# Kernel optimization log

Measured on AMD Instinct MI355X. Metric: run time of the kernel, lower is better.

The kernel has to match this reference:

```python
import jax, jax.numpy as jnp
import numpy as np

M = 8192   # predicted boxes
N = 8192   # ground-truth boxes
W_CENTER, W_SIZE, W_IOU = 1.0, 0.5, 2.0
MATCH_THRESH = 5.0


def setup_inputs() -> dict:
    key = jax.random.key(0)
    k1, k2, k3, k4 = jax.random.split(key, 4)
    centers = jax.random.uniform(k1, (N, 3), dtype=jnp.float32) * 100.0
    sizes = jax.random.uniform(k2, (N, 3), dtype=jnp.float32) * 3.0 + 1.0
    yaw = jax.random.uniform(k3, (N, 1), dtype=jnp.float32) * (2.0 * jnp.pi) - jnp.pi
    gt_boxes = jnp.concatenate([centers, sizes, yaw], axis=1)  # [N,7]
    # preds = perturbed gts so the 5.0 m matching gate actually fires
    pred_boxes = gt_boxes + 0.5 * jax.random.normal(k4, (M, 7), dtype=jnp.float32)
    return {"pred_boxes": pred_boxes, "gt_boxes": gt_boxes}


def _greedy_match(pred_boxes, gt_boxes):
    """Sequential greedy nearest-center matching (torch loop -> lax.scan).
    Column deletion in the original is equivalent to masking with an
    availability vector: argmin over remaining columns with first-tie wins.
    Returns (mask [M] bool: pred i matched, idx [M] int: matched gt index)."""
    # [M,N] center distance matrix (the memory-heavy irregular part)
    diff = pred_boxes[:, None, :3] - gt_boxes[None, :, :3]
    dist = jnp.sqrt(jnp.sum(diff * diff, axis=-1))

    def step(avail, d_row):
        dm = jnp.where(avail, d_row, jnp.inf)
        j = jnp.argmin(dm)
        ok = dm[j] < MATCH_THRESH
        avail = avail.at[j].set(jnp.logical_and(avail[j], jnp.logical_not(ok)))
        return avail, (ok, j)

    avail0 = jnp.ones((gt_boxes.shape[0],), dtype=bool)
    _, (mask, idx) = jax.lax.scan(step, avail0, dist)
    return mask, idx


def _smooth_l1(x):
    a = jnp.abs(x)
    return jnp.where(a < 1.0, 0.5 * a * a, a - 0.5)


def _iou_2d(b1, b2):
    # axis-aligned BEV IoU using (x, y, l, w)
    x1, y1, l1, w1 = b1[:, 0], b1[:, 1], b1[:, 3], b1[:, 4]
    x2, y2, l2, w2 = b2[:, 0], b2[:, 1], b2[:, 3], b2[:, 4]
    iw = jnp.clip(jnp.minimum(x1 + l1 / 2, x2 + l2 / 2) - jnp.maximum(x1 - l1 / 2, x2 - l2 / 2), 0.0)
    ih = jnp.clip(jnp.minimum(y1 + w1 / 2, y2 + w2 / 2) - jnp.maximum(y1 - w1 / 2, y2 - w2 / 2), 0.0)
    inter = iw * ih
    union = l1 * w1 + l2 * w2 - inter
    return inter / (union + 1e-6)


def _loss(pred_boxes, gt_boxes, mask, idx):
    mg = gt_boxes[idx]                              # [M,7] matched gts
    m = mask.astype(pred_boxes.dtype)               # [M]
    k = jnp.maximum(jnp.sum(m), 1.0)                # number of matches
    loss_center = jnp.sum(m[:, None] * _smooth_l1(pred_boxes[:, :3] - mg[:, :3])) / (3.0 * k)
    loss_size = jnp.sum(m[:, None] * _smooth_l1(pred_boxes[:, 3:6] - mg[:, 3:6])) / (3.0 * k)
    d = pred_boxes[:, 6] - mg[:, 6]
    d = jnp.arctan2(jnp.sin(d), jnp.cos(d))         # wrap to (-pi, pi]
    loss_orient = jnp.sum(m * _smooth_l1(d)) / k
    loss_iou = jnp.sum(m * (1.0 - _iou_2d(pred_boxes, mg))) / k
    return W_CENTER * loss_center + W_SIZE * (loss_size + loss_orient) + W_IOU * loss_iou


def reference(pred_boxes, gt_boxes):
    mask, idx = _greedy_match(pred_boxes, gt_boxes)
    return _loss(pred_boxes, gt_boxes, mask, idx)
```

## Files before the change

### kernel.cpp

```cpp
#include <hip/hip_runtime.h>
#include <stdint.h>

#define MROWS 8192
#define NGT   8192
#define KC    8
#define KL    4
#define RPW   2
#define RPL   4
#define THRESH2_BITS 0x41C7FFFFu
#define THRESH_BITS  0x40A00000u

__device__ __forceinline__ unsigned dist2_bits(float px, float py, float pz,
                                               float gx, float gy, float gz) {
#pragma clang fp contract(off)
  float dx = px - gx;
  float dy = py - gy;
  float dz = pz - gz;
  float s = (dx * dx + dy * dy) + dz * dz;
  return __float_as_uint(s);
}

__device__ __forceinline__ unsigned long long wave_min64(unsigned long long v) {
#pragma unroll
  for (int off = 32; off >= 1; off >>= 1) {
    unsigned long long o = __shfl_xor(v, off, 64);
    v = (o < v) ? o : v;
  }
  return v;
}

template <int K>
__device__ __forceinline__ void insert_sorted(unsigned (&kd)[K], unsigned (&ki)[K],
                                              unsigned key, unsigned j) {
#pragma unroll
  for (int t = K - 1; t >= 1; --t) {
    bool a = key < kd[t];
    bool b = key < kd[t - 1];
    if (a) {
      if (b) { kd[t] = kd[t - 1]; ki[t] = ki[t - 1]; }
      else   { kd[t] = key;       ki[t] = j; }
    }
  }
  if (key < kd[0]) { kd[0] = key; ki[0] = j; }
}

template <int K>
__device__ __forceinline__ void extract8(unsigned (&kd)[K], unsigned (&ki)[K], int lane,
                                         unsigned& resd, unsigned& resi,
                                         unsigned long long& e8) {
#pragma unroll
  for (int rr = 0; rr < KC; ++rr) {
    unsigned long long head = ((unsigned long long)kd[0] << 32) | (unsigned long long)ki[0];
    unsigned long long m = wave_min64(head);
    if (head == m) {
#pragma unroll
      for (int t = 0; t < K - 1; ++t) { kd[t] = kd[t + 1]; ki[t] = ki[t + 1]; }
      kd[K - 1] = 0xFFFFFFFFu; ki[K - 1] = 0xFFFFFFFFu;
    }
    if (lane == rr) { resd = (unsigned)(m >> 32); resi = (unsigned)m; }
    e8 = m;
  }
}

__global__ __launch_bounds__(256) void pack_kernel(const float* __restrict__ gt,
                                                   float4* __restrict__ cen) {
  int j = blockIdx.x * 256 + threadIdx.x;
  if (j < NGT) cen[j] = make_float4(gt[j * 7 + 0], gt[j * 7 + 1], gt[j * 7 + 2], 0.0f);
}

__global__ __launch_bounds__(256, 4) void topk_kernel(const float* __restrict__ pred,
                                                      const float4* __restrict__ cen,
                                                      unsigned* __restrict__ cand) {
  const int tid = threadIdx.x;
  const int lane = tid & 63;
  const int wave = (blockIdx.x * 256 + tid) >> 6;
  const int r0 = wave * RPW;

  float px[RPW], py[RPW], pz[RPW];
#pragma unroll
  for (int r = 0; r < RPW; ++r) {
    px[r] = pred[(size_t)(r0 + r) * 7 + 0];
    py[r] = pred[(size_t)(r0 + r) * 7 + 1];
    pz[r] = pred[(size_t)(r0 + r) * 7 + 2];
  }

  unsigned kd[RPW][KL], ki[RPW][KL];
#pragma unroll
  for (int r = 0; r < RPW; ++r)
#pragma unroll
    for (int t = 0; t < KL; ++t) { kd[r][t] = 0xFFFFFFFFu; ki[r][t] = 0xFFFFFFFFu; }

#pragma unroll 2
  for (int j0 = 0; j0 < NGT / 64; ++j0) {
    int j = j0 * 64 + lane;
    float4 c = cen[j];
#pragma unroll
    for (int r = 0; r < RPW; ++r) {
      unsigned key = dist2_bits(px[r], py[r], pz[r], c.x, c.y, c.z);
      if (key < kd[r][KL - 1]) insert_sorted<KL>(kd[r], ki[r], key, (unsigned)j);
    }
  }

#pragma unroll
  for (int r = 0; r < RPW; ++r) {
    const int row = r0 + r;
    unsigned long long guard =
        ((unsigned long long)kd[r][KL - 1] << 32) | (unsigned long long)ki[r][KL - 1];
    unsigned resd = 0, resi = 0;
    unsigned long long e8 = 0;
    extract8<KL>(kd[r], ki[r], lane, resd, resi, e8);

    if (__ballot(guard < e8) != 0ull) {
      unsigned fd[KC], fi[KC];
#pragma unroll
      for (int t = 0; t < KC; ++t) { fd[t] = 0xFFFFFFFFu; fi[t] = 0xFFFFFFFFu; }
      for (int j0 = 0; j0 < NGT / 64; ++j0) {
        int j = j0 * 64 + lane;
        float4 c = cen[j];
        unsigned key = dist2_bits(px[r], py[r], pz[r], c.x, c.y, c.z);
        if (key < fd[KC - 1]) insert_sorted<KC>(fd, fi, key, (unsigned)j);
      }
      unsigned long long dummy;
      extract8<KC>(fd, fi, lane, resd, resi, dummy);
    }
    if (lane < KC)
      cand[(size_t)row * KC + lane] = (resi << 1) | (resd < THRESH2_BITS ? 1u : 0u);
  }
}

__global__ __launch_bounds__(64) void greedy_kernel(const unsigned* __restrict__ cand,
                                                    const float* __restrict__ pred,
                                                    const float* __restrict__ gt,
                                                    unsigned* __restrict__ match) {
  __shared__ unsigned avail[NGT / 32];
  __shared__ unsigned claim[NGT];
  __shared__ float sx[NGT], sy[NGT], sz[NGT];
  const int lane = threadIdx.x;

  for (int w = lane; w < NGT / 32; w += 64) avail[w] = 0xFFFFFFFFu;
  for (int j = lane; j < NGT; j += 64) {
    claim[j] = 0xFFFFFFFFu;
    sx[j] = gt[j * 7 + 0];
    sy[j] = gt[j * 7 + 1];
    sz[j] = gt[j * 7 + 2];
  }
  __syncthreads();

  unsigned ci_[RPL][KC], ni_[RPL][KC];
  int prefBase = -1;

  int base = 0;
  while (base < MROWS) {
    const int nAct = (MROWS - base < 64 * RPL) ? (MROWS - base) : 64 * RPL;

    if (base == prefBase) {
#pragma unroll
      for (int q = 0; q < RPL; ++q)
#pragma unroll
        for (int t = 0; t < KC; ++t) ci_[q][t] = ni_[q][t];
    } else {
#pragma unroll
      for (int q = 0; q < RPL; ++q) {
        int o = lane + 64 * q;
        int r = base + (o < nAct ? o : 0);
        const uint4* cr = (const uint4*)(cand + (size_t)r * KC);
        uint4 a = cr[0], b = cr[1];
        ci_[q][0] = a.x; ci_[q][1] = a.y; ci_[q][2] = a.z; ci_[q][3] = a.w;
        ci_[q][4] = b.x; ci_[q][5] = b.y; ci_[q][6] = b.z; ci_[q][7] = b.w;
      }
    }
    prefBase = base + nAct;
#pragma unroll
    for (int q = 0; q < RPL; ++q) {
      int pr = prefBase + lane + 64 * q;
      if (pr >= MROWS) pr = MROWS - 1;
      const uint4* cr = (const uint4*)(cand + (size_t)pr * KC);
      uint4 a = cr[0], b = cr[1];
      ni_[q][0] = a.x; ni_[q][1] = a.y; ni_[q][2] = a.z; ni_[q][3] = a.w;
      ni_[q][4] = b.x; ni_[q][5] = b.y; ni_[q][6] = b.z; ni_[q][7] = b.w;
    }

    unsigned m[RPL];
#pragma unroll
    for (int q = 0; q < RPL; ++q) {
      int o = lane + 64 * q;
      unsigned mm = 0;
#pragma unroll
      for (int t = 0; t < KC; ++t) {
        unsigned g = ci_[q][t] >> 1;
        mm |= ((avail[g >> 5] >> (g & 31)) & 1u) << t;
      }
      m[q] = (o < nAct) ? mm : 0u;
    }

    unsigned pe[RPL];
    bool cl[RPL];
    bool forceSerial = false;
    int guard = 0;
    while (true) {
#pragma unroll
      for (int q = 0; q < RPL; ++q) {
        unsigned e = 0;
#pragma unroll
        for (int t = KC - 1; t >= 0; --t)
          if (m[q] & (1u << t)) e = ci_[q][t];
        pe[q] = e;
        cl[q] = (m[q] != 0u) && (e & 1u);
      }
#pragma unroll
      for (int q = 0; q < RPL; ++q)
        if (cl[q]) atomicMin(&claim[pe[q] >> 1], (unsigned)(lane + 64 * q));
      __builtin_amdgcn_wave_barrier();
      bool any = false;
      bool lost[RPL];
#pragma unroll
      for (int q = 0; q < RPL; ++q) {
        lost[q] = cl[q] && (claim[pe[q] >> 1] < (unsigned)(lane + 64 * q));
        any |= lost[q];
      }
      if (__ballot(any) == 0ull) break;
#pragma unroll
      for (int q = 0; q < RPL; ++q)
        if (lost[q]) m[q] &= (m[q] - 1u);
      if (++guard > 2100) { forceSerial = true; break; }
    }

    unsigned fe = 1024u;
#pragma unroll
    for (int q = 0; q < RPL; ++q) {
      unsigned o = (unsigned)(lane + 64 * q);
      if (o < (unsigned)nAct && m[q] == 0u && o < fe) fe = o;
    }
#pragma unroll
    for (int off = 32; off >= 1; off >>= 1) {
      unsigned other = __shfl_xor(fe, off, 64);
      fe = other < fe ? other : fe;
    }
    int commitCount = forceSerial ? 0 : ((int)fe < nAct ? (int)fe : nAct);

#pragma unroll
    for (int q = 0; q < RPL; ++q) {
      int o = lane + 64 * q;
      if (o < commitCount) {
        unsigned g = pe[q] >> 1;
        match[base + o] = (cl[q] ? 0x80000000u : 0u) | g;
        if (cl[q]) atomicAnd(&avail[g >> 5], ~(1u << (g & 31)));
      }
    }
#pragma unroll
    for (int q = 0; q < RPL; ++q)
#pragma unroll
      for (int t = 0; t < KC; ++t) claim[ci_[q][t] >> 1] = 0xFFFFFFFFu;
    __builtin_amdgcn_wave_barrier();

    base += commitCount;

    if (commitCount < nAct) {
      const int r = base;
      float fx = pred[(size_t)r * 7 + 0];
      float fy = pred[(size_t)r * 7 + 1];
      float fz = pred[(size_t)r * 7 + 2];
      unsigned long long best = ~0ull;
      for (int j0 = 0; j0 < NGT / 64; ++j0) {
        int j = j0 * 64 + lane;
        if ((avail[j >> 5] >> (j & 31)) & 1u) {
          unsigned db;
          {
#pragma clang fp contract(off)
            float dx = fx - sx[j];
            float dy = fy - sy[j];
            float dz = fz - sz[j];
            float s = (dx * dx + dy * dy) + dz * dz;
            db = __float_as_uint(sqrtf(s));
          }
          unsigned long long key = ((unsigned long long)db << 32) | (unsigned)j;
          if (key < best) best = key;
        }
      }
      unsigned long long mm2 = wave_min64(best);
      if (lane == 0) {
        if (mm2 == ~0ull) {
          match[r] = 0u;
        } else {
          unsigned db = (unsigned)(mm2 >> 32);
          unsigned j = (unsigned)mm2;
          bool ok = db < THRESH_BITS;
          if (ok) atomicAnd(&avail[j >> 5], ~(1u << (j & 31)));
          match[r] = (ok ? 0x80000000u : 0u) | j;
        }
      }
      __builtin_amdgcn_wave_barrier();
      base += 1;
    }
  }
}

__device__ __forceinline__ float smooth_l1(float x) {
  float a = fabsf(x);
  return (a < 1.0f) ? (0.5f * a * a) : (a - 0.5f);
}

__global__ __launch_bounds__(256) void loss_kernel(const float* __restrict__ pred,
                                                   const float* __restrict__ gt,
                                                   const unsigned* __restrict__ match,
                                                   float* __restrict__ acc) {
  int i = blockIdx.x * 256 + threadIdx.x;
  float vc = 0.f, vs = 0.f, vo = 0.f, vi = 0.f, vk = 0.f;
  if (i < MROWS) {
    unsigned r = match[i];
    if (r & 0x80000000u) {
      unsigned j = r & 0x7FFFFFFFu;
      float p[7], g[7];
#pragma unroll
      for (int t = 0; t < 7; ++t) { p[t] = pred[i * 7 + t]; g[t] = gt[j * 7 + t]; }
      vc = smooth_l1(p[0] - g[0]) + smooth_l1(p[1] - g[1]) + smooth_l1(p[2] - g[2]);
      vs = smooth_l1(p[3] - g[3]) + smooth_l1(p[4] - g[4]) + smooth_l1(p[5] - g[5]);
      float d = p[6] - g[6];
      float w = d - 6.283185307179586f * rintf(d * 0.15915494309189535f);
      vo = smooth_l1(w);
      float iw = fminf(p[0] + p[3] * 0.5f, g[0] + g[3] * 0.5f) -
                 fmaxf(p[0] - p[3] * 0.5f, g[0] - g[3] * 0.5f);
      iw = fmaxf(iw, 0.0f);
      float ih = fminf(p[1] + p[4] * 0.5f, g[1] + g[4] * 0.5f) -
                 fmaxf(p[1] - p[4] * 0.5f, g[1] - g[4] * 0.5f);
      ih = fmaxf(ih, 0.0f);
      float inter = iw * ih;
      float uni = p[3] * p[4] + g[3] * g[4] - inter;
      vi = 1.0f - inter / (uni + 1e-6f);
      vk = 1.0f;
    }
  }
#pragma unroll
  for (int off = 32; off >= 1; off >>= 1) {
    vc += __shfl_down(vc, off, 64);
    vs += __shfl_down(vs, off, 64);
    vo += __shfl_down(vo, off, 64);
    vi += __shfl_down(vi, off, 64);
    vk += __shfl_down(vk, off, 64);
  }
  if ((threadIdx.x & 63) == 0) {
    atomicAdd(&acc[0], vc);
    atomicAdd(&acc[1], vs);
    atomicAdd(&acc[2], vo);
    atomicAdd(&acc[3], vi);
    atomicAdd(&acc[4], vk);
  }
}

__global__ void finalize_kernel(const float* __restrict__ acc, float* __restrict__ out) {
  float k = fmaxf(acc[4], 1.0f);
  float loss = acc[0] / (3.0f * k)
             + 0.5f * (acc[1] / (3.0f * k) + acc[2] / k)
             + 2.0f * (acc[3] / k);
  out[0] = loss;
}

extern "C" void kernel_launch(void* const* d_in, const int* in_sizes, int n_in,
                              void* d_out, int out_size, void* d_ws, size_t ws_size,
                              hipStream_t stream) {
  const float* pred = (const float*)d_in[0];
  const float* gt   = (const float*)d_in[1];
  char* ws = (char*)d_ws;
  float* acc       = (float*)ws;
  unsigned* match  = (unsigned*)(ws + 1024);
  unsigned* cand   = (unsigned*)(ws + 33792);
  float4* cen      = (float4*)(ws + 295936);

  hipMemsetAsync(acc, 0, 32, stream);
  pack_kernel<<<NGT / 256, 256, 0, stream>>>(gt, cen);
  topk_kernel<<<MROWS / (RPW * 4), 256, 0, stream>>>(pred, cen, cand);
  greedy_kernel<<<1, 64, 0, stream>>>(cand, pred, gt, match);
  loss_kernel<<<MROWS / 256, 256, 0, stream>>>(pred, gt, match, acc);
  finalize_kernel<<<1, 1, 0, stream>>>(acc, (float*)d_out);
}
```

Before: 214.9 us.

## Resume parallel greedy window after serial fallback instead of restarting window

The greedy matcher now keeps its 256-row window fixed. When a row exhausts its candidates, it runs the full serial scan for that row only, clears the newly taken gt from the other rows' candidate masks, and resumes parallel claiming from the next row. Before, the whole window was rebuilt from the failing row. The serial scan compares squared-distance bits against the squared threshold on packed float4 centers, so it no longer computes a sqrt and no longer needs the shared-memory staging of gt coordinates. The topk kernel drops to one row per wave with a 2-deep local list and higher occupancy, which makes fallback full rescans more likely. The squared-threshold comparison may also differ at exact boundary ties.

```diff
diff --git a/kernel.cpp b/kernel.cpp
--- a/kernel.cpp
+++ b/kernel.cpp
@@ -4,11 +4,9 @@
 #define MROWS 8192
 #define NGT   8192
 #define KC    8
-#define KL    4
-#define RPW   2
+#define KL    2
 #define RPL   4
 #define THRESH2_BITS 0x41C7FFFFu
-#define THRESH_BITS  0x40A00000u
 
 __device__ __forceinline__ unsigned dist2_bits(float px, float py, float pz,
                                                float gx, float gy, float gz) {
@@ -68,111 +66,88 @@
   if (j < NGT) cen[j] = make_float4(gt[j * 7 + 0], gt[j * 7 + 1], gt[j * 7 + 2], 0.0f);
 }
 
-__global__ __launch_bounds__(256, 4) void topk_kernel(const float* __restrict__ pred,
+__global__ __launch_bounds__(256, 8) void topk_kernel(const float* __restrict__ pred,
                                                       const float4* __restrict__ cen,
                                                       unsigned* __restrict__ cand) {
   const int tid = threadIdx.x;
   const int lane = tid & 63;
-  const int wave = (blockIdx.x * 256 + tid) >> 6;
-  const int r0 = wave * RPW;
-
-  float px[RPW], py[RPW], pz[RPW];
-#pragma unroll
-  for (int r = 0; r < RPW; ++r) {
-    px[r] = pred[(size_t)(r0 + r) * 7 + 0];
-    py[r] = pred[(size_t)(r0 + r) * 7 + 1];
-    pz[r] = pred[(size_t)(r0 + r) * 7 + 2];
-  }
-
-  unsigned kd[RPW][KL], ki[RPW][KL];
-#pragma unroll
-  for (int r = 0; r < RPW; ++r)
-#pragma unroll
-    for (int t = 0; t < KL; ++t) { kd[r][t] = 0xFFFFFFFFu; ki[r][t] = 0xFFFFFFFFu; }
+  const int row = (blockIdx.x * 256 + tid) >> 6;
+
+  float px = pred[(size_t)row * 7 + 0];
+  float py = pred[(size_t)row * 7 + 1];
+  float pz = pred[(size_t)row * 7 + 2];
+
+  unsigned kd[KL], ki[KL];
+#pragma unroll
+  for (int t = 0; t < KL; ++t) { kd[t] = 0xFFFFFFFFu; ki[t] = 0xFFFFFFFFu; }
 
 #pragma unroll 2
   for (int j0 = 0; j0 < NGT / 64; ++j0) {
     int j = j0 * 64 + lane;
     float4 c = cen[j];
-#pragma unroll
-    for (int r = 0; r < RPW; ++r) {
-      unsigned key = dist2_bits(px[r], py[r], pz[r], c.x, c.y, c.z);
-      if (key < kd[r][KL - 1]) insert_sorted<KL>(kd[r], ki[r], key, (unsigned)j);
-    }
-  }
-
-#pragma unroll
-  for (int r = 0; r < RPW; ++r) {
-    const int row = r0 + r;
-    unsigned long long guard =
-        ((unsigned long long)kd[r][KL - 1] << 32) | (unsigned long long)ki[r][KL - 1];
-    unsigned resd = 0, resi = 0;
-    unsigned long long e8 = 0;
-    extract8<KL>(kd[r], ki[r], lane, resd, resi, e8);
-
-    if (__ballot(guard < e8) != 0ull) {
-      unsigned fd[KC], fi[KC];
-#pragma unroll
-      for (int t = 0; t < KC; ++t) { fd[t] = 0xFFFFFFFFu; fi[t] = 0xFFFFFFFFu; }
-      for (int j0 = 0; j0 < NGT / 64; ++j0) {
-        int j = j0 * 64 + lane;
-        float4 c = cen[j];
-        unsigned key = dist2_bits(px[r], py[r], pz[r], c.x, c.y, c.z);
-        if (key < fd[KC - 1]) insert_sorted<KC>(fd, fi, key, (unsigned)j);
-      }
-      unsigned long long dummy;
-      extract8<KC>(fd, fi, lane, resd, resi, dummy);
-    }
-    if (lane < KC)
-      cand[(size_t)row * KC + lane] = (resi << 1) | (resd < THRESH2_BITS ? 1u : 0u);
-  }
+    unsigned key = dist2_bits(px, py, pz, c.x, c.y, c.z);
+    if (key < kd[KL - 1]) insert_sorted<KL>(kd, ki, key, (unsigned)j);
+  }
+
+  unsigned long long guard =
+      ((unsigned long long)kd[KL - 1] << 32) | (unsigned long long)ki[KL - 1];
+  unsigned resd = 0, resi = 0;
+  unsigned long long e8 = 0;
+  extract8<KL>(kd, ki, lane, resd, resi, e8);
+
+  if (__ballot(guard < e8) != 0ull) {
+    unsigned fd[KC], fi[KC];
+#pragma unroll
+    for (int t = 0; t < KC; ++t) { fd[t] = 0xFFFFFFFFu; fi[t] = 0xFFFFFFFFu; }
+    for (int j0 = 0; j0 < NGT / 64; ++j0) {
+      int j = j0 * 64 + lane;
+      float4 c = cen[j];
+      unsigned key = dist2_bits(px, py, pz, c.x, c.y, c.z);
+      if (key < fd[KC - 1]) insert_sorted<KC>(fd, fi, key, (unsigned)j);
+    }
+    unsigned long long dummy;
+    extract8<KC>(fd, fi, lane, resd, resi, dummy);
+  }
+  if (lane < KC)
+    cand[(size_t)row * KC + lane] = (resi << 1) | (resd < THRESH2_BITS ? 1u : 0u);
 }
 
 __global__ __launch_bounds__(64) void greedy_kernel(const unsigned* __restrict__ cand,
                                                     const float* __restrict__ pred,
-                                                    const float* __restrict__ gt,
+                                                    const float4* __restrict__ cen,
                                                     unsigned* __restrict__ match) {
   __shared__ unsigned avail[NGT / 32];
   __shared__ unsigned claim[NGT];
-  __shared__ float sx[NGT], sy[NGT], sz[NGT];
   const int lane = threadIdx.x;
 
   for (int w = lane; w < NGT / 32; w += 64) avail[w] = 0xFFFFFFFFu;
-  for (int j = lane; j < NGT; j += 64) {
-    claim[j] = 0xFFFFFFFFu;
-    sx[j] = gt[j * 7 + 0];
-    sy[j] = gt[j * 7 + 1];
-    sz[j] = gt[j * 7 + 2];
-  }
+  for (int j = lane; j < NGT; j += 64) claim[j] = 0xFFFFFFFFu;
   __syncthreads();
 
   unsigned ci_[RPL][KC], ni_[RPL][KC];
-  int prefBase = -1;
-
-  int base = 0;
-  while (base < MROWS) {
-    const int nAct = (MROWS - base < 64 * RPL) ? (MROWS - base) : 64 * RPL;
-
-    if (base == prefBase) {
-#pragma unroll
-      for (int q = 0; q < RPL; ++q)
-#pragma unroll
-        for (int t = 0; t < KC; ++t) ci_[q][t] = ni_[q][t];
-    } else {
+  bool first = true;
+
+  for (int base = 0; base < MROWS; base += 64 * RPL) {
+    const int nAct = 64 * RPL;
+
+    if (first) {
 #pragma unroll
       for (int q = 0; q < RPL; ++q) {
-        int o = lane + 64 * q;
-        int r = base + (o < nAct ? o : 0);
-        const uint4* cr = (const uint4*)(cand + (size_t)r * KC);
+        const uint4* cr = (const uint4*)(cand + (size_t)(base + lane + 64 * q) * KC);
         uint4 a = cr[0], b = cr[1];
         ci_[q][0] = a.x; ci_[q][1] = a.y; ci_[q][2] = a.z; ci_[q][3] = a.w;
         ci_[q][4] = b.x; ci_[q][5] = b.y; ci_[q][6] = b.z; ci_[q][7] = b.w;
       }
-    }
-    prefBase = base + nAct;
+      first = false;
+    } else {
+#pragma unroll
+      for (int q = 0; q < RPL; ++q)
+#pragma unroll
+        for (int t = 0; t < KC; ++t) ci_[q][t] = ni_[q][t];
+    }
 #pragma unroll
     for (int q = 0; q < RPL; ++q) {
-      int pr = prefBase + lane + 64 * q;
+      int pr = base + nAct + lane + 64 * q;
       if (pr >= MROWS) pr = MROWS - 1;
       const uint4* cr = (const uint4*)(cand + (size_t)pr * KC);
       uint4 a = cr[0], b = cr[1];
@@ -183,115 +158,126 @@
     unsigned m[RPL];
 #pragma unroll
     for (int q = 0; q < RPL; ++q) {
-      int o = lane + 64 * q;
       unsigned mm = 0;
 #pragma unroll
       for (int t = 0; t < KC; ++t) {
         unsigned g = ci_[q][t] >> 1;
         mm |= ((avail[g >> 5] >> (g & 31)) & 1u) << t;
       }
-      m[q] = (o < nAct) ? mm : 0u;
-    }
-
+      m[q] = mm;
+    }
+
+    int floor_ = 0;
     unsigned pe[RPL];
     bool cl[RPL];
-    bool forceSerial = false;
-    int guard = 0;
+    int rounds = 0;
+
     while (true) {
+      while (true) {
+#pragma unroll
+        for (int q = 0; q < RPL; ++q) {
+          int o = lane + 64 * q;
+          unsigned e = 0;
+#pragma unroll
+          for (int t = KC - 1; t >= 0; --t)
+            if (m[q] & (1u << t)) e = ci_[q][t];
+          pe[q] = e;
+          cl[q] = (o >= floor_) && (m[q] != 0u) && (e & 1u);
+        }
+#pragma unroll
+        for (int q = 0; q < RPL; ++q)
+          if (cl[q]) atomicMin(&claim[pe[q] >> 1], (unsigned)(lane + 64 * q));
+        __builtin_amdgcn_wave_barrier();
+        bool any = false;
+        bool lost[RPL];
+#pragma unroll
+        for (int q = 0; q < RPL; ++q) {
+          lost[q] = cl[q] && (claim[pe[q] >> 1] < (unsigned)(lane + 64 * q));
+          any |= lost[q];
+        }
+        if (__ballot(any) == 0ull) break;
+#pragma unroll
+        for (int q = 0; q < RPL; ++q)
+          if (lost[q]) m[q] &= (m[q] - 1u);
+        if (++rounds > 2100) {
+#pragma unroll
+          for (int q = 0; q < RPL; ++q)
+            if (lane + 64 * q >= floor_) m[q] = 0u;
+        }
+      }
+
+      unsigned fe = 0xFFFFu;
 #pragma unroll
       for (int q = 0; q < RPL; ++q) {
-        unsigned e = 0;
-#pragma unroll
-        for (int t = KC - 1; t >= 0; --t)
-          if (m[q] & (1u << t)) e = ci_[q][t];
-        pe[q] = e;
-        cl[q] = (m[q] != 0u) && (e & 1u);
-      }
-#pragma unroll
-      for (int q = 0; q < RPL; ++q)
-        if (cl[q]) atomicMin(&claim[pe[q] >> 1], (unsigned)(lane + 64 * q));
+        unsigned o = (unsigned)(lane + 64 * q);
+        if (o >= (unsigned)floor_ && m[q] == 0u && o < fe) fe = o;
+      }
+#pragma unroll
+      for (int off = 32; off >= 1; off >>= 1) {
+        unsigned o2 = __shfl_xor(fe, off, 64);
+        fe = o2 < fe ? o2 : fe;
+      }
+      int feI = (fe == 0xFFFFu) ? nAct : (int)fe;
+
+#pragma unroll
+      for (int q = 0; q < RPL; ++q) {
+        int o = lane + 64 * q;
+        if (o >= floor_ && o < feI) {
+          unsigned g = pe[q] >> 1;
+          match[base + o] = (cl[q] ? 0x80000000u : 0u) | g;
+          if (cl[q]) atomicAnd(&avail[g >> 5], ~(1u << (g & 31)));
+        }
+      }
       __builtin_amdgcn_wave_barrier();
-      bool any = false;
-      bool lost[RPL];
-#pragma unroll
-      for (int q = 0; q < RPL; ++q) {
-        lost[q] = cl[q] && (claim[pe[q] >> 1] < (unsigned)(lane + 64 * q));
-        any |= lost[q];
-      }
-      if (__ballot(any) == 0ull) break;
-#pragma unroll
-      for (int q = 0; q < RPL; ++q)
-        if (lost[q]) m[q] &= (m[q] - 1u);
-      if (++guard > 2100) { forceSerial = true; break; }
-    }
-
-    unsigned fe = 1024u;
-#pragma unroll
-    for (int q = 0; q < RPL; ++q) {
-      unsigned o = (unsigned)(lane + 64 * q);
-      if (o < (unsigned)nAct && m[q] == 0u && o < fe) fe = o;
-    }
-#pragma unroll
-    for (int off = 32; off >= 1; off >>= 1) {
-      unsigned other = __shfl_xor(fe, off, 64);
-      fe = other < fe ? other : fe;
-    }
-    int commitCount = forceSerial ? 0 : ((int)fe < nAct ? (int)fe : nAct);
-
-#pragma unroll
-    for (int q = 0; q < RPL; ++q) {
-      int o = lane + 64 * q;
-      if (o < commitCount) {
-        unsigned g = pe[q] >> 1;
-        match[base + o] = (cl[q] ? 0x80000000u : 0u) | g;
-        if (cl[q]) atomicAnd(&avail[g >> 5], ~(1u << (g & 31)));
-      }
-    }
+      if (feI == nAct) break;
+
+      {
+        const int r = base + feI;
+        float fx = pred[(size_t)r * 7 + 0];
+        float fy = pred[(size_t)r * 7 + 1];
+        float fz = pred[(size_t)r * 7 + 2];
+        unsigned long long best = ~0ull;
+        for (int j0 = 0; j0 < NGT / 64; ++j0) {
+          int j = j0 * 64 + lane;
+          if ((avail[j >> 5] >> (j & 31)) & 1u) {
+            float4 c = cen[j];
+            unsigned sb = dist2_bits(fx, fy, fz, c.x, c.y, c.z);
+            unsigned long long key = ((unsigned long long)sb << 32) | (unsigned)j;
+            if (key < best) best = key;
+          }
+        }
+        unsigned long long mm2 = wave_min64(best);
+        unsigned gstar = 0xFFFFFFFFu;
+        if (mm2 != ~0ull) {
+          unsigned sb = (unsigned)(mm2 >> 32);
+          unsigned j = (unsigned)mm2;
+          bool ok = sb < THRESH2_BITS;
+          if (lane == 0) {
+            match[r] = (ok ? 0x80000000u : 0u) | j;
+            if (ok) atomicAnd(&avail[j >> 5], ~(1u << (j & 31)));
+          }
+          if (ok) gstar = j;
+        } else if (lane == 0) {
+          match[r] = 0u;
+        }
+        __builtin_amdgcn_wave_barrier();
+        if (gstar != 0xFFFFFFFFu) {
+#pragma unroll
+          for (int q = 0; q < RPL; ++q)
+#pragma unroll
+            for (int t = 0; t < KC; ++t)
+              if ((ci_[q][t] >> 1) == gstar) m[q] &= ~(1u << t);
+        }
+        floor_ = feI + 1;
+        if (floor_ >= nAct) break;
+      }
+    }
+
 #pragma unroll
     for (int q = 0; q < RPL; ++q)
 #pragma unroll
       for (int t = 0; t < KC; ++t) claim[ci_[q][t] >> 1] = 0xFFFFFFFFu;
     __builtin_amdgcn_wave_barrier();
-
-    base += commitCount;
-
-    if (commitCount < nAct) {
-      const int r = base;
-      float fx = pred[(size_t)r * 7 + 0];
-      float fy = pred[(size_t)r * 7 + 1];
-      float fz = pred[(size_t)r * 7 + 2];
-      unsigned long long best = ~0ull;
-      for (int j0 = 0; j0 < NGT / 64; ++j0) {
-        int j = j0 * 64 + lane;
-        if ((avail[j >> 5] >> (j & 31)) & 1u) {
-          unsigned db;
-          {
-#pragma clang fp contract(off)
-            float dx = fx - sx[j];
-            float dy = fy - sy[j];
-            float dz = fz - sz[j];
-            float s = (dx * dx + dy * dy) + dz * dz;
-            db = __float_as_uint(sqrtf(s));
-          }
-          unsigned long long key = ((unsigned long long)db << 32) | (unsigned)j;
-          if (key < best) best = key;
-        }
-      }
-      unsigned long long mm2 = wave_min64(best);
-      if (lane == 0) {
-        if (mm2 == ~0ull) {
-          match[r] = 0u;
-        } else {
-          unsigned db = (unsigned)(mm2 >> 32);
-          unsigned j = (unsigned)mm2;
-          bool ok = db < THRESH_BITS;
-          if (ok) atomicAnd(&avail[j >> 5], ~(1u << (j & 31)));
-          match[r] = (ok ? 0x80000000u : 0u) | j;
-        }
-      }
-      __builtin_amdgcn_wave_barrier();
-      base += 1;
-    }
   }
 }
 
@@ -368,8 +354,8 @@
 
   hipMemsetAsync(acc, 0, 32, stream);
   pack_kernel<<<NGT / 256, 256, 0, stream>>>(gt, cen);
-  topk_kernel<<<MROWS / (RPW * 4), 256, 0, stream>>>(pred, cen, cand);
-  greedy_kernel<<<1, 64, 0, stream>>>(cand, pred, gt, match);
+  topk_kernel<<<MROWS / 4, 256, 0, stream>>>(pred, cen, cand);
+  greedy_kernel<<<1, 64, 0, stream>>>(cand, pred, cen, match);
   loss_kernel<<<MROWS / 256, 256, 0, stream>>>(pred, gt, match, acc);
   finalize_kernel<<<1, 1, 0, stream>>>(acc, (float*)d_out);
 }
```

Measured after the change: 258.1 us. 20.1% more time.
